# Optimization experiments

Hardware: AMD Instinct MI355X
Metric: run time of the kernel (lower is better)

Reference implementation:

```python
import jax, jax.numpy as jnp
import numpy as np

EXP = 1.4  # cp/cv exponent in the pressure diagnostic

# 2-point stencil primitives (equivalent to the tiny conv3d calls in the torch code)
def bar_x(X):      return 0.5 * (X[:, :, 1:] + X[:, :, :-1])
def dlt_x(X, dx):  return (X[:, :, 1:] - X[:, :, :-1]) / dx
def bar_y(X):      return 0.5 * (X[:, 1:, :] + X[:, :-1, :])
def dlt_y(X, dy):  return (X[:, 1:, :] - X[:, :-1, :]) / dy
def bar_z(X):      return 0.5 * (X[1:] + X[:-1])
def dlt_z(X, dz):  return (X[1:] - X[:-1]) / dz
def pad_x(X):      return jnp.pad(X, ((0, 0), (0, 0), (1, 1)), mode='wrap')      # periodic
def pad_y(X):      return jnp.pad(X, ((0, 0), (1, 1), (0, 0)), mode='wrap')      # periodic
def pad_z(X):      return jnp.pad(X, ((1, 1), (0, 0), (0, 0)))                   # Dirichlet 0 (torch code zeroes top/surface args)


def rhs(U, V, W, Theta, Mu, Phi, dx, dy, dz, PREF, Rd, g):
    u = U / bar_x(pad_x(Mu))                       # (Nz,Ny,Nx+1)
    v = V / bar_y(pad_y(Mu))                       # (Nz,Ny+1,Nx)
    w = W / bar_z(Mu)                              # (Nz-1,Ny,Nx)
    alpha = -dlt_z(pad_z(Phi), dz) / Mu            # (Nz,Ny,Nx)
    theta = Theta / Mu
    p = PREF * (Rd * theta / PREF / alpha) ** EXP
    omega = -w * g / bar_z(alpha) / bar_z(Mu)
    Omega = omega * bar_z(Mu)                      # (Nz-1,Ny,Nx)

    R_U = (-dlt_x(bar_x(pad_x(U)) * bar_x(pad_x(u)), dx)
           - dlt_y(bar_x(pad_x(V)) * bar_y(pad_y(u)), dy)
           - dlt_z(bar_x(pad_x(pad_z(Omega))) * bar_z(pad_z(u)), dz))
    R_V = (-dlt_x(bar_y(pad_y(U)) * bar_x(pad_x(v)), dx)
           - dlt_y(bar_y(pad_y(V)) * bar_y(pad_y(v)), dy)
           - dlt_z(bar_y(pad_y(pad_z(Omega))) * bar_z(pad_z(v)), dz))
    R_W = (-dlt_x(bar_z(U) * bar_x(pad_x(w)), dx)
           - dlt_y(bar_z(V) * bar_y(pad_y(w)), dy)
           - dlt_z(bar_z(pad_z(Omega)) * bar_z(pad_z(w)), dz))
    R_Theta = (-dlt_x(U * bar_x(pad_x(theta)), dx)
               - dlt_y(V * bar_y(pad_y(theta)), dy)
               - dlt_z(pad_z(Omega) * bar_z(pad_z(theta)), dz))
    R_Phi = (-bar_z(bar_x(u)) * dlt_x(bar_x(pad_x(Phi)), dx)
             - bar_z(bar_y(v)) * dlt_y(bar_y(pad_y(Phi)), dy)
             - Omega * dlt_z(bar_z(pad_z(Phi)), dz))
    R_Mu = -dlt_x(U, dx) - dlt_y(V, dy) - dlt_z(pad_z(Omega), dz)

    R_U = R_U + (-bar_x(pad_x(Mu)) * bar_x(pad_x(alpha)) * dlt_x(pad_x(p), dx)
                 - dlt_z(bar_x(bar_z(pad_x(pad_z(p)))), dz) * dlt_x(pad_x(bar_z(pad_z(Phi))), dx))
    R_V = R_V + (-bar_y(pad_y(Mu)) * bar_y(pad_y(alpha)) * dlt_y(pad_y(p), dy)
                 - dlt_z(bar_y(bar_z(pad_y(pad_z(p)))), dz) * dlt_y(pad_y(bar_z(pad_z(Phi))), dy))
    R_W = R_W + g * (dlt_z(p, dz) - bar_z(Mu))
    R_Phi = R_Phi + g * w
    return R_U, R_V, R_W, R_Theta, R_Mu, R_Phi


def rk3_step(U, V, W, Theta, Mu, Phi, dt, dx, dy, dz, PREF, Rd, g):
    rU, rV, rW, rT, rM, rP = rhs(U, V, W, Theta, Mu, Phi, dx, dy, dz, PREF, Rd, g)
    U1, V1, W1 = U + dt * rU / 3, V + dt * rV / 3, W + dt * rW / 3
    T1, M1, P1 = Theta + dt * rT / 3, Mu + dt * rM / 3, Phi + dt * rP / 3
    rU, rV, rW, rT, rM, rP = rhs(U1, V1, W1, T1, M1, P1, dx, dy, dz, PREF, Rd, g)
    U2, V2, W2 = U + dt * rU / 2, V + dt * rV / 2, W + dt * rW / 2
    T2, M2, P2 = Theta + dt * rT / 2, Mu + dt * rM / 2, Phi + dt * rP / 2
    rU, rV, rW, rT, rM, rP = rhs(U2, V2, W2, T2, M2, P2, dx, dy, dz, PREF, Rd, g)
    return (U + dt * rU, V + dt * rV, W + dt * rW,
            Theta + dt * rT, Mu + dt * rM, Phi + dt * rP)


def setup_inputs() -> dict:
    Nz, Ny, Nx = 40, 256, 256
    key = jax.random.key(0)
    k1, k2, k3, k4, k5, k6, k7 = jax.random.split(key, 7)
    dx = dy = dz = 1.0
    dt, PREF, Rd, g = 1e-3, 1.0, 1.0, 0.1

    # Column-mass: positive, O(1)
    Mu = (1.0 + 0.1 * jax.random.uniform(k1, (Nz, Ny, Nx))).astype(jnp.float32)
    # Block-signed vertical diff profile: magnitudes bounded away from 0,
    # distinct block magnitudes so bar_z(alpha) never vanishes at the sign flip.
    base = jnp.where(jnp.arange(Nz) < 30, 1.0, -3.0)[:, None, None]
    d = (base * (1.0 + 0.1 * jax.random.uniform(k2, (Nz, Ny, Nx)))).astype(jnp.float32)
    Phi = jnp.cumsum(d, axis=0)[: Nz - 1]          # (Nz-1,Ny,Nx)
    # alpha exactly as the model will compute it
    alpha = -dlt_z(pad_z(Phi), dz) / Mu            # (Nz,Ny,Nx), sign-definite per block
    s = 1.0 + 0.2 * jax.random.uniform(k3, (Nz, Ny, Nx))
    Theta = ((PREF / Rd) * Mu * alpha * s).astype(jnp.float32)  # theta/alpha = s > 0 -> p well-defined

    U = (0.01 * jax.random.normal(k4, (Nz, Ny, Nx + 1))).astype(jnp.float32)
    V = (0.01 * jax.random.normal(k5, (Nz, Ny + 1, Nx))).astype(jnp.float32)
    W = (0.01 * jax.random.normal(k6, (Nz - 1, Ny, Nx))).astype(jnp.float32)

    bnd = jax.random.uniform(k7, (6, 1, Ny, Nx), dtype=jnp.float32)
    return {"U": U, "V": V, "W": W, "Theta": Theta, "Mu": Mu, "Phi": Phi,
            "Phi_t": bnd[0], "Phi_s": bnd[1], "theta_t": bnd[2], "theta_s": bnd[3],
            "P_t": bnd[4], "P_s": bnd[5],
            "dx": dx, "dy": dy, "dz": dz, "dt": dt, "PREF": PREF, "Rd": Rd, "g": g}


def reference(U, V, W, Theta, Mu, Phi, Phi_t, Phi_s, theta_t, theta_s, P_t, P_s,
              dx, dy, dz, dt, PREF, Rd, g):
    # Phi_t/Phi_s/theta_t/theta_s/P_t/P_s are ignored: the torch pad_z always
    # overwrites top/surface with zeros (faithful to the original code).
    return rk3_step(U, V, W, Theta, Mu, Phi, dt, dx, dy, dz, PREF, Rd, g)
```

## Files before the change

### kernel.cpp

```cpp
#include <hip/hip_runtime.h>
#include <math.h>

#define NZ 40
#define NY 256
#define NX 256
#define NUX 257
#define NYX (NY*NX)
#define KU (NY*NUX)
#define KV ((NY+1)*NX)
#define NUT (NZ*KU)
#define NVT (NZ*KV)
#define NCT (NZ*NYX)
#define NWT ((NZ-1)*NYX)
#define NBLK (NUX*NZ)

__device__ __forceinline__ int ICc(int k,int j,int i){ return (k*NY+j)*NX+i; }
__device__ __forceinline__ int IU (int k,int j,int i){ return (k*NY+j)*NUX+i; }
__device__ __forceinline__ int IV (int k,int j,int i){ return (k*(NY+1)+j)*NX+i; }

__device__ __forceinline__ float fdiv(float a, float b){
  return a * __builtin_amdgcn_rcpf(b);
}

__device__ __forceinline__ float u_at(const float* __restrict__ Us, const float* __restrict__ Ms,
                                      int k,int j,int i){
  const int ii = i & 255, im = (i+255) & 255;
  const int b = (k*NY+j)*NX;
  return fdiv(Us[(k*NY+j)*NUX+i], 0.5f*(Ms[b+im]+Ms[b+ii]));
}
__device__ __forceinline__ float v_at(const float* __restrict__ Vs, const float* __restrict__ Ms,
                                      int k,int j,int i){
  const int jj = j & 255, jm = (j+255) & 255;
  return fdiv(Vs[(k*(NY+1)+j)*NX+i], 0.5f*(Ms[(k*NY+jm)*NX+i]+Ms[(k*NY+jj)*NX+i]));
}
__device__ __forceinline__ float w_at(const float* __restrict__ Ws, const float* __restrict__ Ms,
                                      int k,int j,int i){
  const int c = (k*NY+j)*NX+i;
  return fdiv(Ws[c], 0.5f*(Ms[c]+Ms[c+NYX]));
}
__device__ __forceinline__ float th_at(const float* __restrict__ Ts, const float* __restrict__ Ms,
                                       int k,int j,int i){
  const int c = (k*NY+j)*NX+i;
  return fdiv(Ts[c], Ms[c]);
}

__global__ __launch_bounds__(256) void diag_pOm(
    const float* __restrict__ Ws, const float* __restrict__ Ts,
    const float* __restrict__ Ms, const float* __restrict__ Ps,
    float* __restrict__ pd, float* __restrict__ Omd, float* __restrict__ ald,
    const float* __restrict__ dzp, const float* __restrict__ PREFp,
    const float* __restrict__ Rdp, const float* __restrict__ gp)
{
  const int i = threadIdx.x, j = blockIdx.x, k = blockIdx.y;
  const float rdz = 1.f/(*dzp);
  const float PREF = *PREFp, Rd = *Rdp, g = *gp;
  const float invP = 1.f/PREF;
  const int c = ICc(k,j,i);
  float mu   = Ms[c];
  float phim = (k>0)    ? Ps[c-NYX] : 0.f;
  float phik = (k<NZ-1) ? Ps[c]     : 0.f;
  float al   = -((phik-phim)*rdz)/mu;
  float th   = Ts[c]/mu;
  pd[c]  = PREF*powf(Rd*th*invP/al, 1.4f);
  ald[c] = al;
  if (k < NZ-1) {
    float mup  = Ms[c+NYX];
    float phip = (k+1<NZ-1) ? Ps[c+NYX] : 0.f;
    float alp  = -((phip-phik)*rdz)/mup;
    Omd[c] = -Ws[c]*g/((0.5f*(mu+mup))*(0.5f*(al+alp)));
  }
}

__device__ __forceinline__ float ru_val(int k,int j,int i,int iW,int iE,
    const float* __restrict__ Us, const float* __restrict__ Vs,
    const float* __restrict__ Ms, const float* __restrict__ Ps,
    const float* __restrict__ pd, const float* __restrict__ Omd,
    const float* __restrict__ ald,
    float rdx, float rdy, float rdz)
{
  const int ii  = i & 255;
  const int im1 = (i+255) & 255;
  const int jm1 = (j+255) & 255;
  const int jpm = (j+1) & 255;
  const int bU  = k*KU + j*NUX;

  float ui0 = u_at(Us,Ms,k,j,i);
  float uim = u_at(Us,Ms,k,j,iW);
  float uip = u_at(Us,Ms,k,j,iE);
  float Uim = Us[bU+iW], Ui0 = Us[bU+i], Uip = Us[bU+iE];
  float t1 = -(0.25f*(Ui0+Uip)*(ui0+uip) - 0.25f*(Uim+Ui0)*(uim+ui0))*rdx;

  float Vx0 = 0.5f*(Vs[IV(k,j  ,im1)] + Vs[IV(k,j  ,ii)]);
  float uy0 = 0.5f*(u_at(Us,Ms,k,jm1,i) + ui0);
  float Vx1 = 0.5f*(Vs[IV(k,j+1,im1)] + Vs[IV(k,j+1,ii)]);
  float uy1 = 0.5f*(ui0 + u_at(Us,Ms,k,jpm,i));
  float t2 = -(Vx1*uy1 - Vx0*uy0)*rdy;

  float Omx0 = (k==0)   ? 0.f : 0.5f*(Omd[ICc(k-1,j,im1)]+Omd[ICc(k-1,j,ii)]);
  float uz0  = (k==0)   ? 0.5f*ui0 : 0.5f*(u_at(Us,Ms,k-1,j,i)+ui0);
  float Omx1 = (k+1==NZ)? 0.f : 0.5f*(Omd[ICc(k,j,im1)]+Omd[ICc(k,j,ii)]);
  float uz1  = (k+1==NZ)? 0.5f*ui0 : 0.5f*(ui0+u_at(Us,Ms,k+1,j,i));
  float t3 = -(Omx1*uz1 - Omx0*uz0)*rdz;

  float Mux = 0.5f*(Ms[ICc(k,j,im1)]+Ms[ICc(k,j,ii)]);
  float alx = 0.5f*(ald[ICc(k,j,im1)]+ald[ICc(k,j,ii)]);
  float pt1 = -Mux*alx*(pd[ICc(k,j,ii)]-pd[ICc(k,j,im1)])*rdx;

  auto pzf = [&](int m, int x)->float {
    if (m==0)  return 0.5f*pd[ICc(0,j,x)];
    if (m==NZ) return 0.5f*pd[ICc(NZ-1,j,x)];
    return 0.5f*(pd[ICc(m-1,j,x)]+pd[ICc(m,j,x)]);
  };
  float A = (0.5f*(pzf(k+1,im1)+pzf(k+1,ii)) - 0.5f*(pzf(k,im1)+pzf(k,ii)))*rdz;
  auto Phzf = [&](int x)->float {
    if (k==0)    return 0.5f*Ps[ICc(0,j,x)];
    if (k==NZ-1) return 0.5f*Ps[ICc(NZ-2,j,x)];
    return 0.5f*(Ps[ICc(k-1,j,x)]+Ps[ICc(k,j,x)]);
  };
  float B = (Phzf(ii)-Phzf(im1))*rdx;
  return t1+t2+t3+pt1 + (-A*B);
}

__global__ __launch_bounds__(256,8) void rhs_update(
    const float* __restrict__ Us, const float* __restrict__ Vs, const float* __restrict__ Ws,
    const float* __restrict__ Ts, const float* __restrict__ Ms, const float* __restrict__ Ps,
    const float* __restrict__ pd, const float* __restrict__ Omd, const float* __restrict__ ald,
    const float* __restrict__ Ub, const float* __restrict__ Vb, const float* __restrict__ Wb,
    const float* __restrict__ Tb, const float* __restrict__ Mb, const float* __restrict__ Pb,
    float* __restrict__ Uo, float* __restrict__ Vo, float* __restrict__ Wo,
    float* __restrict__ To, float* __restrict__ Mo, float* __restrict__ Po,
    const float* __restrict__ dxp, const float* __restrict__ dyp, const float* __restrict__ dzp,
    const float* __restrict__ dtp, const float* __restrict__ gp, float cmul)
{
  const int bid = blockIdx.x;
  const int nb  = (bid & 7)*(NBLK/8) + (bid >> 3);
  const int j   = nb / NZ;
  const int k   = nb - NZ*j;
  const int i   = threadIdx.x;

  const float rdx = 1.f/(*dxp), rdy = 1.f/(*dyp), rdz = 1.f/(*dzp);
  const float g = *gp;
  const float c = (*dtp)*cmul;

  const int jj  = j & 255;
  const int jm1 = (j+255) & 255;
  const int im1 = (i+255) & 255;
  const int ip1 = (i+1) & 255;

  if (j < NY) {
    const int iW = i ? (i-1) : 256;
    float rU = ru_val(k,j,i, iW, i+1, Us,Vs,Ms,Ps, pd,Omd,ald, rdx,rdy,rdz);
    const int o = IU(k,j,i);
    Uo[o] = Ub[o] + c*rU;
    if (i == 255) {
      float rUe = ru_val(k,j,256, 255, 0, Us,Vs,Ms,Ps, pd,Omd,ald, rdx,rdy,rdz);
      const int oe = IU(k,j,256);
      Uo[oe] = Ub[oe] + c*rUe;
    }
  }

  {
    const int jN = (j==0)   ? 256 : j-1;
    const int jS = (j==256) ? 0   : j+1;
    float vj0 = v_at(Vs,Ms,k,j,i);
    float vjm = v_at(Vs,Ms,k,jN,i);
    float vjp = v_at(Vs,Ms,k,jS,i);
    float Vjm = Vs[IV(k,jN,i)], Vj0 = Vs[IV(k,j,i)], Vjp = Vs[IV(k,jS,i)];
    float t2 = -(0.25f*(Vj0+Vjp)*(vj0+vjp) - 0.25f*(Vjm+Vj0)*(vjm+vj0))*rdy;

    float Uy0 = 0.5f*(Us[IU(k,jm1,i  )] + Us[IU(k,jj,i  )]);
    float vx0 = 0.5f*(v_at(Vs,Ms,k,j,im1) + vj0);
    float Uy1 = 0.5f*(Us[IU(k,jm1,i+1)] + Us[IU(k,jj,i+1)]);
    float vx1 = 0.5f*(vj0 + v_at(Vs,Ms,k,j,ip1));
    float t1 = -(Uy1*vx1 - Uy0*vx0)*rdx;

    float Omy0 = (k==0)   ? 0.f : 0.5f*(Omd[ICc(k-1,jm1,i)]+Omd[ICc(k-1,jj,i)]);
    float vz0  = (k==0)   ? 0.5f*vj0 : 0.5f*(v_at(Vs,Ms,k-1,j,i)+vj0);
    float Omy1 = (k+1==NZ)? 0.f : 0.5f*(Omd[ICc(k,jm1,i)]+Omd[ICc(k,jj,i)]);
    float vz1  = (k+1==NZ)? 0.5f*vj0 : 0.5f*(vj0+v_at(Vs,Ms,k+1,j,i));
    float t3 = -(Omy1*vz1 - Omy0*vz0)*rdz;

    float Muy = 0.5f*(Ms[ICc(k,jm1,i)]+Ms[ICc(k,jj,i)]);
    float aly = 0.5f*(ald[ICc(k,jm1,i)]+ald[ICc(k,jj,i)]);
    float pt1 = -Muy*aly*(pd[ICc(k,jj,i)]-pd[ICc(k,jm1,i)])*rdy;

    auto pzfy = [&](int m, int y)->float {
      if (m==0)  return 0.5f*pd[ICc(0,y,i)];
      if (m==NZ) return 0.5f*pd[ICc(NZ-1,y,i)];
      return 0.5f*(pd[ICc(m-1,y,i)]+pd[ICc(m,y,i)]);
    };
    float A = (0.5f*(pzfy(k+1,jm1)+pzfy(k+1,jj)) - 0.5f*(pzfy(k,jm1)+pzfy(k,jj)))*rdz;
    auto Phzfy = [&](int y)->float {
      if (k==0)    return 0.5f*Ps[ICc(0,y,i)];
      if (k==NZ-1) return 0.5f*Ps[ICc(NZ-2,y,i)];
      return 0.5f*(Ps[ICc(k-1,y,i)]+Ps[ICc(k,y,i)]);
    };
    float B = (Phzfy(jj)-Phzfy(jm1))*rdy;
    float pt2 = -A*B;

    const int o = IV(k,j,i);
    Vo[o] = Vb[o] + c*(t1+t2+t3+pt1+pt2);
  }

  if (j < NY) {
    const int cc = ICc(k,j,i);
    const int jp1 = (j+1)&255;

    float th0 = th_at(Ts,Ms,k,j,i);
    float thx0 = 0.5f*(th_at(Ts,Ms,k,j,im1)+th0);
    float thx1 = 0.5f*(th0+th_at(Ts,Ms,k,j,ip1));
    float s1 = -(Us[IU(k,j,i+1)]*thx1 - Us[IU(k,j,i)]*thx0)*rdx;
    float thy0 = 0.5f*(th_at(Ts,Ms,k,jm1,i)+th0);
    float thy1 = 0.5f*(th0+th_at(Ts,Ms,k,jp1,i));
    float s2 = -(Vs[IV(k,j+1,i)]*thy1 - Vs[IV(k,j,i)]*thy0)*rdy;
    float Om0 = (k==0)    ? 0.f : Omd[ICc(k-1,j,i)];
    float Om1 = (k+1==NZ) ? 0.f : Omd[cc];
    float thz0 = (k==0)    ? 0.5f*th0 : 0.5f*(th_at(Ts,Ms,k-1,j,i)+th0);
    float thz1 = (k+1==NZ) ? 0.5f*th0 : 0.5f*(th0+th_at(Ts,Ms,k+1,j,i));
    float s3 = -(Om1*thz1 - Om0*thz0)*rdz;
    To[cc] = Tb[cc] + c*(s1+s2+s3);

    float rmu = -(Us[IU(k,j,i+1)]-Us[IU(k,j,i)])*rdx
                -(Vs[IV(k,j+1,i)]-Vs[IV(k,j,i)])*rdy
                -(Om1-Om0)*rdz;
    Mo[cc] = Mb[cc] + c*rmu;

    if (k < NZ-1) {
      float w0 = w_at(Ws,Ms,k,j,i);
      float Uz0 = 0.5f*(Us[IU(k,j,i  )]+Us[IU(k+1,j,i  )]);
      float Uz1 = 0.5f*(Us[IU(k,j,i+1)]+Us[IU(k+1,j,i+1)]);
      float wx0 = 0.5f*(w_at(Ws,Ms,k,j,im1)+w0);
      float wx1 = 0.5f*(w0+w_at(Ws,Ms,k,j,ip1));
      float q1 = -(Uz1*wx1 - Uz0*wx0)*rdx;
      float Vz0 = 0.5f*(Vs[IV(k,j  ,i)]+Vs[IV(k+1,j  ,i)]);
      float Vz1 = 0.5f*(Vs[IV(k,j+1,i)]+Vs[IV(k+1,j+1,i)]);
      float wy0 = 0.5f*(w_at(Ws,Ms,k,jm1,i)+w0);
      float wy1 = 0.5f*(w0+w_at(Ws,Ms,k,jp1,i));
      float q2 = -(Vz1*wy1 - Vz0*wy0)*rdy;
      float Omz0 = (k==0)      ? 0.5f*Omd[ICc(0,j,i)]    : 0.5f*(Omd[ICc(k-1,j,i)]+Omd[cc]);
      float wz0  = (k==0)      ? 0.5f*w0 : 0.5f*(w_at(Ws,Ms,k-1,j,i)+w0);
      float Omz1 = (k+1==NZ-1) ? 0.5f*Omd[ICc(NZ-2,j,i)] : 0.5f*(Omd[cc]+Omd[ICc(k+1,j,i)]);
      float wz1  = (k+1==NZ-1) ? 0.5f*w0 : 0.5f*(w0+w_at(Ws,Ms,k+1,j,i));
      float q3 = -(Omz1*wz1 - Omz0*wz0)*rdz;
      float pw = g*((pd[ICc(k+1,j,i)]-pd[cc])*rdz - 0.5f*(Ms[cc]+Ms[ICc(k+1,j,i)]));
      Wo[cc] = Wb[cc] + c*(q1+q2+q3+pw);

      float ux0 = 0.5f*(u_at(Us,Ms,k  ,j,i)+u_at(Us,Ms,k  ,j,i+1));
      float ux1 = 0.5f*(u_at(Us,Ms,k+1,j,i)+u_at(Us,Ms,k+1,j,i+1));
      float uzx = 0.5f*(ux0+ux1);
      float dPhx = 0.5f*(Ps[ICc(k,j,ip1)]-Ps[ICc(k,j,im1)])*rdx;
      float vy0 = 0.5f*(v_at(Vs,Ms,k  ,j,i)+v_at(Vs,Ms,k  ,j+1,i));
      float vy1 = 0.5f*(v_at(Vs,Ms,k+1,j,i)+v_at(Vs,Ms,k+1,j+1,i));
      float vzy = 0.5f*(vy0+vy1);
      float dPhy = 0.5f*(Ps[ICc(k,jp1,i)]-Ps[ICc(k,jm1,i)])*rdy;
      float Phz0 = (k==0)      ? 0.5f*Ps[ICc(0,j,i)]    : 0.5f*(Ps[ICc(k-1,j,i)]+Ps[cc]);
      float Phz1 = (k+1==NZ-1) ? 0.5f*Ps[ICc(NZ-2,j,i)] : 0.5f*(Ps[cc]+Ps[ICc(k+1,j,i)]);
      float p3 = -Omd[cc]*(Phz1-Phz0)*rdz;
      Po[cc] = Pb[cc] + c*(-uzx*dPhx - vzy*dPhy + p3 + g*w0);
    }
  }
}

extern "C" void kernel_launch(void* const* d_in, const int* in_sizes, int n_in,
                              void* d_out, int out_size, void* d_ws, size_t ws_size,
                              hipStream_t stream)
{
  const float* U = (const float*)d_in[0];
  const float* V = (const float*)d_in[1];
  const float* W = (const float*)d_in[2];
  const float* T = (const float*)d_in[3];
  const float* M = (const float*)d_in[4];
  const float* P = (const float*)d_in[5];
  const float* dxp  = (const float*)d_in[12];
  const float* dyp  = (const float*)d_in[13];
  const float* dzp  = (const float*)d_in[14];
  const float* dtp  = (const float*)d_in[15];
  const float* PREFp= (const float*)d_in[16];
  const float* Rdp  = (const float*)d_in[17];
  const float* gp   = (const float*)d_in[18];

  float* ws = (float*)d_ws;
  float* pd  = ws;
  float* Omd = pd  + NCT;
  float* ald = Omd + NWT;
  float* S   = ald + NCT;
  float* SU=S; float* SV=SU+NUT; float* SW=SV+NVT; float* ST=SW+NWT; float* SM=ST+NCT; float* SP=SM+NCT;

  float* o = (float*)d_out;
  float* OU=o; float* OV=OU+NUT; float* OW=OV+NVT; float* OT=OW+NWT; float* OM=OT+NCT; float* OP=OM+NCT;

  dim3 blk(256,1,1);
  dim3 dgrd(NY, NZ, 1);
  dim3 rgrd(NBLK, 1, 1);

  auto stage = [&](const float* sU,const float* sV,const float* sW,
                   const float* sT,const float* sM,const float* sP,
                   float* oU,float* oV,float* oW,float* oT,float* oM,float* oP,
                   float cmul){
    hipLaunchKernelGGL(diag_pOm, dgrd, blk, 0, stream,
                       sW,sT,sM,sP, pd,Omd,ald, dzp,PREFp,Rdp,gp);
    hipLaunchKernelGGL(rhs_update, rgrd, blk, 0, stream,
                       sU,sV,sW,sT,sM,sP, pd,Omd,ald,
                       U,V,W,T,M,P, oU,oV,oW,oT,oM,oP,
                       dxp,dyp,dzp,dtp,gp, cmul);
  };

  stage(U,V,W,T,M,P,          OU,OV,OW,OT,OM,OP, 1.f/3.f);
  stage(OU,OV,OW,OT,OM,OP,    SU,SV,SW,ST,SM,SP, 0.5f   );
  stage(SU,SV,SW,ST,SM,SP,    OU,OV,OW,OT,OM,OP, 1.f    );
}
```

Before: 319.8 us.

## March RHS kernel over vertical chunks with register-rotated z-neighbour reuse

Each block of the RHS/update kernel now handles one (j) row across a chunk of 8 vertical levels instead of a single level. Vertically adjacent values (u, v, w, theta, Omega, p, Phi and their west/north neighbours) are held in registers and rotated as k advances, so each level's z-stencil inputs are loaded once rather than three times. The grid shrinks by a factor of 8, and launch bounds drop to 4 waves per SIMD to allow more registers. The cost is fewer blocks (1285), serial dependence within a chunk, higher register pressure and lower occupancy, which may hide latency less well on a memory-bound kernel.

Measured after the change: 502.4 us. 1.57x slower.

```diff
diff --git a/kernel.cpp b/kernel.cpp
--- a/kernel.cpp
+++ b/kernel.cpp
@@ -12,7 +12,9 @@
 #define NVT (NZ*KV)
 #define NCT (NZ*NYX)
 #define NWT ((NZ-1)*NYX)
-#define NBLK (NUX*NZ)
+#define NCH 5
+#define KCH 8
+#define NBLK2 (NUX*NCH)
 
 __device__ __forceinline__ int ICc(int k,int j,int i){ return (k*NY+j)*NX+i; }
 __device__ __forceinline__ int IU (int k,int j,int i){ return (k*NY+j)*NUX+i; }
@@ -71,7 +73,7 @@
   }
 }
 
-__device__ __forceinline__ float ru_val(int k,int j,int i,int iW,int iE,
+__device__ __forceinline__ float ru_edge(int k,int j,int i,int iW,int iE,
     const float* __restrict__ Us, const float* __restrict__ Vs,
     const float* __restrict__ Ms, const float* __restrict__ Ps,
     const float* __restrict__ pd, const float* __restrict__ Omd,
@@ -80,8 +82,8 @@
 {
   const int ii  = i & 255;
   const int im1 = (i+255) & 255;
-  const int jm1 = (j+255) & 255;
-  const int jpm = (j+1) & 255;
+  const int jm1 = (j+255)&255;
+  const int jpm = (j+1)&255;
   const int bU  = k*KU + j*NUX;
 
   float ui0 = u_at(Us,Ms,k,j,i);
@@ -121,7 +123,7 @@
   return t1+t2+t3+pt1 + (-A*B);
 }
 
-__global__ __launch_bounds__(256,8) void rhs_update(
+__global__ __launch_bounds__(256,4) void rhs_march(
     const float* __restrict__ Us, const float* __restrict__ Vs, const float* __restrict__ Ws,
     const float* __restrict__ Ts, const float* __restrict__ Ms, const float* __restrict__ Ps,
     const float* __restrict__ pd, const float* __restrict__ Omd, const float* __restrict__ ald,
@@ -133,131 +135,168 @@
     const float* __restrict__ dtp, const float* __restrict__ gp, float cmul)
 {
   const int bid = blockIdx.x;
-  const int nb  = (bid & 7)*(NBLK/8) + (bid >> 3);
-  const int j   = nb / NZ;
-  const int k   = nb - NZ*j;
-  const int i   = threadIdx.x;
+  const int q = NBLK2/8, r = NBLK2%8;
+  const int xcd = bid & 7, pos = bid >> 3;
+  const int nb = (xcd<r ? xcd*(q+1) : r*(q+1)+(xcd-r)*q) + pos;
+  const int kc = nb / NUX;
+  const int j  = nb - kc*NUX;
+  const int k0 = kc*KCH;
+  const int i  = threadIdx.x;
+
+  const bool doC = (j < NY);
+  const int jc  = j & 255;
+  const int jm1 = (j+255) & 255;
+  const int jp1 = (jc+1) & 255;
+  const int im1 = (i+255) & 255;
+  const int ip1 = (i+1) & 255;
+  const int iW  = i ? (i-1) : 256;
+  const int jN  = (j==0)   ? 256 : j-1;
+  const int jS  = (j==256) ? 0   : j+1;
 
   const float rdx = 1.f/(*dxp), rdy = 1.f/(*dyp), rdz = 1.f/(*dzp);
   const float g = *gp;
   const float c = (*dtp)*cmul;
 
-  const int jj  = j & 255;
-  const int jm1 = (j+255) & 255;
-  const int im1 = (i+255) & 255;
-  const int ip1 = (i+1) & 255;
-
-  if (j < NY) {
-    const int iW = i ? (i-1) : 256;
-    float rU = ru_val(k,j,i, iW, i+1, Us,Vs,Ms,Ps, pd,Omd,ald, rdx,rdy,rdz);
-    const int o = IU(k,j,i);
-    Uo[o] = Ub[o] + c*rU;
-    if (i == 255) {
-      float rUe = ru_val(k,j,256, 255, 0, Us,Vs,Ms,Ps, pd,Omd,ald, rdx,rdy,rdz);
-      const int oe = IU(k,j,256);
-      Uo[oe] = Ub[oe] + c*rUe;
+  auto F_u  = [&](int m)->float { return (doC && (unsigned)m < NZ  ) ? u_at (Us,Ms,m,j,i)    : 0.f; };
+  auto F_uE = [&](int m)->float { return (doC && (unsigned)m < NZ  ) ? u_at (Us,Ms,m,j,i+1)  : 0.f; };
+  auto F_v  = [&](int m)->float { return (       (unsigned)m < NZ  ) ? v_at (Vs,Ms,m,j,i)    : 0.f; };
+  auto F_vS = [&](int m)->float { return (doC && (unsigned)m < NZ  ) ? v_at (Vs,Ms,m,j+1,i)  : 0.f; };
+  auto F_w  = [&](int m)->float { return (doC && (unsigned)m < NZ-1) ? w_at (Ws,Ms,m,j,i)    : 0.f; };
+  auto F_th = [&](int m)->float { return (doC && (unsigned)m < NZ  ) ? th_at(Ts,Ms,m,j,i)    : 0.f; };
+  auto F_Om = [&](int m)->float { return (       (unsigned)m < NZ-1) ? Omd[(m*NY+jm1==jm1?(m*NY+jc)*NX+i:(m*NY+jc)*NX+i)] : 0.f; };
+  auto F_OmW= [&](int m)->float { return (doC && (unsigned)m < NZ-1) ? Omd[(m*NY+j  )*NX+im1] : 0.f; };
+  auto F_OmN= [&](int m)->float { return (       (unsigned)m < NZ-1) ? Omd[(m*NY+jm1)*NX+i  ] : 0.f; };
+  auto F_p  = [&](int m)->float { return (       (unsigned)m < NZ  ) ? pd [(m*NY+jc )*NX+i  ] : 0.f; };
+  auto F_pW = [&](int m)->float { return (doC && (unsigned)m < NZ  ) ? pd [(m*NY+j  )*NX+im1] : 0.f; };
+  auto F_pN = [&](int m)->float { return (       (unsigned)m < NZ  ) ? pd [(m*NY+jm1)*NX+i  ] : 0.f; };
+  auto F_Ph = [&](int m)->float { return (       (unsigned)m < NZ-1) ? Ps [(m*NY+jc )*NX+i  ] : 0.f; };
+  auto F_PhW= [&](int m)->float { return (doC && (unsigned)m < NZ-1) ? Ps [(m*NY+j  )*NX+im1] : 0.f; };
+  auto F_PhN= [&](int m)->float { return (       (unsigned)m < NZ-1) ? Ps [(m*NY+jm1)*NX+i  ] : 0.f; };
+
+  float uCm=F_u(k0-1),  uCc=F_u(k0),  uCp=F_u(k0+1);
+  float uEc=F_uE(k0),   uEp=F_uE(k0+1);
+  float vCm=F_v(k0-1),  vCc=F_v(k0),  vCp=F_v(k0+1);
+  float vSc=F_vS(k0),   vSp=F_vS(k0+1);
+  float wCm=F_w(k0-1),  wCc=F_w(k0),  wCp=F_w(k0+1);
+  float thCm=F_th(k0-1),thCc=F_th(k0),thCp=F_th(k0+1);
+  float OmCm=F_Om(k0-1),OmCc=F_Om(k0),OmCp=F_Om(k0+1);
+  float OmWm=F_OmW(k0-1),OmWc=F_OmW(k0);
+  float OmNm=F_OmN(k0-1),OmNc=F_OmN(k0);
+  float pCm=F_p(k0-1),  pCc=F_p(k0),  pCp=F_p(k0+1);
+  float pWm=F_pW(k0-1), pWc=F_pW(k0), pWp=F_pW(k0+1);
+  float pNm=F_pN(k0-1), pNc=F_pN(k0), pNp=F_pN(k0+1);
+  float PhCm=F_Ph(k0-1),PhCc=F_Ph(k0),PhCp=F_Ph(k0+1);
+  float PhWm=F_PhW(k0-1),PhWc=F_PhW(k0);
+  float PhNm=F_PhN(k0-1),PhNc=F_PhN(k0);
+
+  for (int k = k0; k < k0+KCH; ++k) {
+    const int cc = (k*NY+jc)*NX+i;
+
+    float UsC0 = Us[(k*NY+jc )*NUX+i];
+    float UsC1 = Us[(k*NY+jc )*NUX+i+1];
+    float UsN0 = Us[(k*NY+jm1)*NUX+i];
+    float UsN1 = Us[(k*NY+jm1)*NUX+i+1];
+    float VsC  = Vs[IV(k,j ,i)];
+    float VsS  = Vs[IV(k,jS,i)];
+    float VsN  = Vs[IV(k,jN,i)];
+    float MsC  = Ms[(k*NY+jc )*NX+i];
+    float MsN  = Ms[(k*NY+jm1)*NX+i];
+    float alC  = ald[(k*NY+jc )*NX+i];
+    float alN  = ald[(k*NY+jm1)*NX+i];
+
+    {
+      float vjm = v_at(Vs,Ms,k,jN,i);
+      float vjp = doC ? vSc : v_at(Vs,Ms,k,jS,i);
+      float t2v = -(0.25f*(VsC+VsS)*(vCc+vjp) - 0.25f*(VsN+VsC)*(vjm+vCc))*rdy;
+      float vx0 = 0.5f*(v_at(Vs,Ms,k,j,im1) + vCc);
+      float vx1 = 0.5f*(vCc + v_at(Vs,Ms,k,j,ip1));
+      float Uy0 = 0.5f*(UsN0+UsC0);
+      float Uy1 = 0.5f*(UsN1+UsC1);
+      float t1v = -(Uy1*vx1 - Uy0*vx0)*rdx;
+      float t3v = -(0.5f*(OmNc+OmCc)*(0.5f*(vCc+vCp)) - 0.5f*(OmNm+OmCm)*(0.5f*(vCm+vCc)))*rdz;
+      float pt1v= -(0.5f*(MsN+MsC))*(0.5f*(alN+alC))*(pCc-pNc)*rdy;
+      float Ay  = 0.25f*rdz*((pNp-pNm)+(pCp-pCm));
+      float By  = 0.5f*rdy*((PhCm+PhCc)-(PhNm+PhNc));
+      const int ov = IV(k,j,i);
+      Vo[ov] = Vb[ov] + c*(t1v+t2v+t3v+pt1v - Ay*By);
     }
-  }
-
-  {
-    const int jN = (j==0)   ? 256 : j-1;
-    const int jS = (j==256) ? 0   : j+1;
-    float vj0 = v_at(Vs,Ms,k,j,i);
-    float vjm = v_at(Vs,Ms,k,jN,i);
-    float vjp = v_at(Vs,Ms,k,jS,i);
-    float Vjm = Vs[IV(k,jN,i)], Vj0 = Vs[IV(k,j,i)], Vjp = Vs[IV(k,jS,i)];
-    float t2 = -(0.25f*(Vj0+Vjp)*(vj0+vjp) - 0.25f*(Vjm+Vj0)*(vjm+vj0))*rdy;
-
-    float Uy0 = 0.5f*(Us[IU(k,jm1,i  )] + Us[IU(k,jj,i  )]);
-    float vx0 = 0.5f*(v_at(Vs,Ms,k,j,im1) + vj0);
-    float Uy1 = 0.5f*(Us[IU(k,jm1,i+1)] + Us[IU(k,jj,i+1)]);
-    float vx1 = 0.5f*(vj0 + v_at(Vs,Ms,k,j,ip1));
-    float t1 = -(Uy1*vx1 - Uy0*vx0)*rdx;
-
-    float Omy0 = (k==0)   ? 0.f : 0.5f*(Omd[ICc(k-1,jm1,i)]+Omd[ICc(k-1,jj,i)]);
-    float vz0  = (k==0)   ? 0.5f*vj0 : 0.5f*(v_at(Vs,Ms,k-1,j,i)+vj0);
-    float Omy1 = (k+1==NZ)? 0.f : 0.5f*(Omd[ICc(k,jm1,i)]+Omd[ICc(k,jj,i)]);
-    float vz1  = (k+1==NZ)? 0.5f*vj0 : 0.5f*(vj0+v_at(Vs,Ms,k+1,j,i));
-    float t3 = -(Omy1*vz1 - Omy0*vz0)*rdz;
-
-    float Muy = 0.5f*(Ms[ICc(k,jm1,i)]+Ms[ICc(k,jj,i)]);
-    float aly = 0.5f*(ald[ICc(k,jm1,i)]+ald[ICc(k,jj,i)]);
-    float pt1 = -Muy*aly*(pd[ICc(k,jj,i)]-pd[ICc(k,jm1,i)])*rdy;
-
-    auto pzfy = [&](int m, int y)->float {
-      if (m==0)  return 0.5f*pd[ICc(0,y,i)];
-      if (m==NZ) return 0.5f*pd[ICc(NZ-1,y,i)];
-      return 0.5f*(pd[ICc(m-1,y,i)]+pd[ICc(m,y,i)]);
-    };
-    float A = (0.5f*(pzfy(k+1,jm1)+pzfy(k+1,jj)) - 0.5f*(pzfy(k,jm1)+pzfy(k,jj)))*rdz;
-    auto Phzfy = [&](int y)->float {
-      if (k==0)    return 0.5f*Ps[ICc(0,y,i)];
-      if (k==NZ-1) return 0.5f*Ps[ICc(NZ-2,y,i)];
-      return 0.5f*(Ps[ICc(k-1,y,i)]+Ps[ICc(k,y,i)]);
-    };
-    float B = (Phzfy(jj)-Phzfy(jm1))*rdy;
-    float pt2 = -A*B;
-
-    const int o = IV(k,j,i);
-    Vo[o] = Vb[o] + c*(t1+t2+t3+pt1+pt2);
-  }
-
-  if (j < NY) {
-    const int cc = ICc(k,j,i);
-    const int jp1 = (j+1)&255;
-
-    float th0 = th_at(Ts,Ms,k,j,i);
-    float thx0 = 0.5f*(th_at(Ts,Ms,k,j,im1)+th0);
-    float thx1 = 0.5f*(th0+th_at(Ts,Ms,k,j,ip1));
-    float s1 = -(Us[IU(k,j,i+1)]*thx1 - Us[IU(k,j,i)]*thx0)*rdx;
-    float thy0 = 0.5f*(th_at(Ts,Ms,k,jm1,i)+th0);
-    float thy1 = 0.5f*(th0+th_at(Ts,Ms,k,jp1,i));
-    float s2 = -(Vs[IV(k,j+1,i)]*thy1 - Vs[IV(k,j,i)]*thy0)*rdy;
-    float Om0 = (k==0)    ? 0.f : Omd[ICc(k-1,j,i)];
-    float Om1 = (k+1==NZ) ? 0.f : Omd[cc];
-    float thz0 = (k==0)    ? 0.5f*th0 : 0.5f*(th_at(Ts,Ms,k-1,j,i)+th0);
-    float thz1 = (k+1==NZ) ? 0.5f*th0 : 0.5f*(th0+th_at(Ts,Ms,k+1,j,i));
-    float s3 = -(Om1*thz1 - Om0*thz0)*rdz;
-    To[cc] = Tb[cc] + c*(s1+s2+s3);
-
-    float rmu = -(Us[IU(k,j,i+1)]-Us[IU(k,j,i)])*rdx
-                -(Vs[IV(k,j+1,i)]-Vs[IV(k,j,i)])*rdy
-                -(Om1-Om0)*rdz;
-    Mo[cc] = Mb[cc] + c*rmu;
-
-    if (k < NZ-1) {
-      float w0 = w_at(Ws,Ms,k,j,i);
-      float Uz0 = 0.5f*(Us[IU(k,j,i  )]+Us[IU(k+1,j,i  )]);
-      float Uz1 = 0.5f*(Us[IU(k,j,i+1)]+Us[IU(k+1,j,i+1)]);
-      float wx0 = 0.5f*(w_at(Ws,Ms,k,j,im1)+w0);
-      float wx1 = 0.5f*(w0+w_at(Ws,Ms,k,j,ip1));
-      float q1 = -(Uz1*wx1 - Uz0*wx0)*rdx;
-      float Vz0 = 0.5f*(Vs[IV(k,j  ,i)]+Vs[IV(k+1,j  ,i)]);
-      float Vz1 = 0.5f*(Vs[IV(k,j+1,i)]+Vs[IV(k+1,j+1,i)]);
-      float wy0 = 0.5f*(w_at(Ws,Ms,k,jm1,i)+w0);
-      float wy1 = 0.5f*(w0+w_at(Ws,Ms,k,jp1,i));
-      float q2 = -(Vz1*wy1 - Vz0*wy0)*rdy;
-      float Omz0 = (k==0)      ? 0.5f*Omd[ICc(0,j,i)]    : 0.5f*(Omd[ICc(k-1,j,i)]+Omd[cc]);
-      float wz0  = (k==0)      ? 0.5f*w0 : 0.5f*(w_at(Ws,Ms,k-1,j,i)+w0);
-      float Omz1 = (k+1==NZ-1) ? 0.5f*Omd[ICc(NZ-2,j,i)] : 0.5f*(Omd[cc]+Omd[ICc(k+1,j,i)]);
-      float wz1  = (k+1==NZ-1) ? 0.5f*w0 : 0.5f*(w0+w_at(Ws,Ms,k+1,j,i));
-      float q3 = -(Omz1*wz1 - Omz0*wz0)*rdz;
-      float pw = g*((pd[ICc(k+1,j,i)]-pd[cc])*rdz - 0.5f*(Ms[cc]+Ms[ICc(k+1,j,i)]));
-      Wo[cc] = Wb[cc] + c*(q1+q2+q3+pw);
-
-      float ux0 = 0.5f*(u_at(Us,Ms,k  ,j,i)+u_at(Us,Ms,k  ,j,i+1));
-      float ux1 = 0.5f*(u_at(Us,Ms,k+1,j,i)+u_at(Us,Ms,k+1,j,i+1));
-      float uzx = 0.5f*(ux0+ux1);
-      float dPhx = 0.5f*(Ps[ICc(k,j,ip1)]-Ps[ICc(k,j,im1)])*rdx;
-      float vy0 = 0.5f*(v_at(Vs,Ms,k  ,j,i)+v_at(Vs,Ms,k  ,j+1,i));
-      float vy1 = 0.5f*(v_at(Vs,Ms,k+1,j,i)+v_at(Vs,Ms,k+1,j+1,i));
-      float vzy = 0.5f*(vy0+vy1);
-      float dPhy = 0.5f*(Ps[ICc(k,jp1,i)]-Ps[ICc(k,jm1,i)])*rdy;
-      float Phz0 = (k==0)      ? 0.5f*Ps[ICc(0,j,i)]    : 0.5f*(Ps[ICc(k-1,j,i)]+Ps[cc]);
-      float Phz1 = (k+1==NZ-1) ? 0.5f*Ps[ICc(NZ-2,j,i)] : 0.5f*(Ps[cc]+Ps[ICc(k+1,j,i)]);
-      float p3 = -Omd[cc]*(Phz1-Phz0)*rdz;
-      Po[cc] = Pb[cc] + c*(-uzx*dPhx - vzy*dPhy + p3 + g*w0);
+
+    if (doC) {
+      const int bU = k*KU + j*NUX;
+      {
+        float Uim = Us[bU+iW];
+        float uim = u_at(Us,Ms,k,j,iW);
+        float t1 = -(0.25f*(UsC0+UsC1)*(uCc+uEc) - 0.25f*(Uim+UsC0)*(uim+uCc))*rdx;
+        float Vx0 = 0.5f*(Vs[IV(k,j  ,im1)] + VsC);
+        float Vx1 = 0.5f*(Vs[IV(k,j+1,im1)] + VsS);
+        float uy0 = 0.5f*(u_at(Us,Ms,k,jm1,i) + uCc);
+        float uy1 = 0.5f*(uCc + u_at(Us,Ms,k,jp1,i));
+        float t2 = -(Vx1*uy1 - Vx0*uy0)*rdy;
+        float t3 = -(0.5f*(OmWc+OmCc)*(0.5f*(uCc+uCp)) - 0.5f*(OmWm+OmCm)*(0.5f*(uCm+uCc)))*rdz;
+        float MsW = Ms[(k*NY+j)*NX+im1];
+        float alW = ald[(k*NY+j)*NX+im1];
+        float pt1 = -(0.5f*(MsW+MsC))*(0.5f*(alW+alC))*(pCc-pWc)*rdx;
+        float A = 0.25f*rdz*((pWp-pWm)+(pCp-pCm));
+        float B = 0.5f*rdx*((PhCm+PhCc)-(PhWm+PhWc));
+        const int o = bU+i;
+        Uo[o] = Ub[o] + c*(t1+t2+t3+pt1 - A*B);
+        if (i == 255) {
+          float rUe = ru_edge(k,j,256, 255, 0, Us,Vs,Ms,Ps, pd,Omd,ald, rdx,rdy,rdz);
+          const int oe = bU+256;
+          Uo[oe] = Ub[oe] + c*rUe;
+        }
+      }
+      {
+        float thx0 = 0.5f*(th_at(Ts,Ms,k,j,im1)+thCc);
+        float thx1 = 0.5f*(thCc+th_at(Ts,Ms,k,j,ip1));
+        float s1 = -(UsC1*thx1 - UsC0*thx0)*rdx;
+        float thy0 = 0.5f*(th_at(Ts,Ms,k,jm1,i)+thCc);
+        float thy1 = 0.5f*(thCc+th_at(Ts,Ms,k,jp1,i));
+        float s2 = -(VsS*thy1 - VsC*thy0)*rdy;
+        float s3 = -(OmCc*(0.5f*(thCc+thCp)) - OmCm*(0.5f*(thCm+thCc)))*rdz;
+        To[cc] = Tb[cc] + c*(s1+s2+s3);
+        float rmu = -(UsC1-UsC0)*rdx - (VsS-VsC)*rdy - (OmCc-OmCm)*rdz;
+        Mo[cc] = Mb[cc] + c*rmu;
+      }
+      if (k < NZ-1) {
+        float Uz0 = 0.5f*(UsC0 + Us[((k+1)*NY+j)*NUX+i  ]);
+        float Uz1 = 0.5f*(UsC1 + Us[((k+1)*NY+j)*NUX+i+1]);
+        float wx0 = 0.5f*(w_at(Ws,Ms,k,j,im1)+wCc);
+        float wx1 = 0.5f*(wCc+w_at(Ws,Ms,k,j,ip1));
+        float q1 = -(Uz1*wx1 - Uz0*wx0)*rdx;
+        float Vz0 = 0.5f*(VsC + Vs[IV(k+1,j  ,i)]);
+        float Vz1 = 0.5f*(VsS + Vs[IV(k+1,j+1,i)]);
+        float wy0 = 0.5f*(w_at(Ws,Ms,k,jm1,i)+wCc);
+        float wy1 = 0.5f*(wCc+w_at(Ws,Ms,k,jp1,i));
+        float q2 = -(Vz1*wy1 - Vz0*wy0)*rdy;
+        float q3 = -(0.5f*(OmCc+OmCp)*(0.5f*(wCc+wCp)) - 0.5f*(OmCm+OmCc)*(0.5f*(wCm+wCc)))*rdz;
+        float pw = g*((pCp-pCc)*rdz - 0.5f*(MsC + Ms[((k+1)*NY+j)*NX+i]));
+        Wo[cc] = Wb[cc] + c*(q1+q2+q3+pw);
+
+        float uzx = 0.25f*((uCc+uEc)+(uCp+uEp));
+        float dPhx = 0.5f*(Ps[(k*NY+j)*NX+ip1] - PhWc)*rdx;
+        float vzy = 0.25f*((vCc+vSc)+(vCp+vSp));
+        float dPhy = 0.5f*(Ps[(k*NY+jp1)*NX+i] - PhNc)*rdy;
+        float p3 = -OmCc*(0.5f*(PhCp-PhCm))*rdz;
+        Po[cc] = Pb[cc] + c*(-uzx*dPhx - vzy*dPhy + p3 + g*wCc);
+      }
     }
+
+    uCm=uCc;  uCc=uCp;  uCp=F_u(k+2);
+    uEc=uEp;  uEp=F_uE(k+2);
+    vCm=vCc;  vCc=vCp;  vCp=F_v(k+2);
+    vSc=vSp;  vSp=F_vS(k+2);
+    wCm=wCc;  wCc=wCp;  wCp=F_w(k+2);
+    thCm=thCc;thCc=thCp;thCp=F_th(k+2);
+    OmCm=OmCc;OmCc=OmCp;OmCp=F_Om(k+2);
+    OmWm=OmWc;OmWc=F_OmW(k+1);
+    OmNm=OmNc;OmNc=F_OmN(k+1);
+    pCm=pCc;  pCc=pCp;  pCp=F_p(k+2);
+    pWm=pWc;  pWc=pWp;  pWp=F_pW(k+2);
+    pNm=pNc;  pNc=pNp;  pNp=F_pN(k+2);
+    PhCm=PhCc;PhCc=PhCp;PhCp=F_Ph(k+2);
+    PhWm=PhWc;PhWc=F_PhW(k+1);
+    PhNm=PhNc;PhNc=F_PhN(k+1);
   }
 }
 
@@ -291,7 +330,7 @@
 
   dim3 blk(256,1,1);
   dim3 dgrd(NY, NZ, 1);
-  dim3 rgrd(NBLK, 1, 1);
+  dim3 rgrd(NBLK2, 1, 1);
 
   auto stage = [&](const float* sU,const float* sV,const float* sW,
                    const float* sT,const float* sM,const float* sP,
@@ -299,7 +338,7 @@
                    float cmul){
     hipLaunchKernelGGL(diag_pOm, dgrd, blk, 0, stream,
                        sW,sT,sM,sP, pd,Omd,ald, dzp,PREFp,Rdp,gp);
-    hipLaunchKernelGGL(rhs_update, rgrd, blk, 0, stream,
+    hipLaunchKernelGGL(rhs_march, rgrd, blk, 0, stream,
                        sU,sV,sW,sT,sM,sP, pd,Omd,ald,
                        U,V,W,T,M,P, oU,oV,oW,oT,oM,oP,
                        dxp,dyp,dzp,dtp,gp, cmul);
```
